# Kernel optimization log

Measured on AMD Instinct MI355X. Metric: run time of the kernel, lower is better.

## Reference

```python
import jax, jax.numpy as jnp
import numpy as np

N = 50000          # num nodes
E = 256            # expert_hidden_dim
H = 512            # hidden_dim (expert output / GNN dim)
NE = 5             # num experts: action, spatial, temporal, semantic, safety
K = 2              # top_k
GH = 128           # gating hidden dim
EDGES = 800000
L = 2              # gnn layers
TEMP = 1.0


def setup_inputs() -> dict:
    key = jax.random.key(0)
    ks = jax.random.split(key, 16)
    s = 0.02
    inp = {
        "text": jax.random.normal(ks[0], (N, E), jnp.float32),
        "tabular": jax.random.normal(ks[1], (N, E), jnp.float32),
        "structured": jax.random.normal(ks[2], (N, E), jnp.float32),
        "edge_index": jax.random.randint(ks[3], (2, EDGES), 0, N, jnp.int64),
        # gating MLP: [3E] -> GH -> NE
        "Wg1": jax.random.normal(ks[4], (3 * E, GH), jnp.float32) * s,
        "bg1": jnp.zeros((GH,), jnp.float32),
        "Wg2": jax.random.normal(ks[5], (GH, NE), jnp.float32) * s,
        "bg2": jnp.zeros((NE,), jnp.float32),
        # 5 expert MLPs (stacked): E -> H -> H
        "We1": jax.random.normal(ks[6], (NE, E, H), jnp.float32) * s,
        "be1": jnp.zeros((NE, H), jnp.float32),
        "We2": jax.random.normal(ks[7], (NE, H, H), jnp.float32) * s,
        "be2": jnp.zeros((NE, H), jnp.float32),
        # GNN per-layer self/neighbor transforms
        "Wself": jax.random.normal(ks[8], (L, H, H), jnp.float32) * s,
        "Wnbr": jax.random.normal(ks[9], (L, H, H), jnp.float32) * s,
    }
    return inp


def _moe_gnn(text, tabular, structured, edge_index,
             Wg1, bg1, Wg2, bg2, We1, be1, We2, be2, Wself, Wnbr):
    # ---- gating: softmax over experts, top-k, renormalize ----
    combined = jnp.concatenate([text, tabular, structured], axis=-1)  # [N, 3E]
    g = jax.nn.relu(combined @ Wg1 + bg1)
    logits = (g @ Wg2 + bg2) / TEMP                                   # [N, NE]
    probs = jax.nn.softmax(logits, axis=-1)
    top_vals, top_idx = jax.lax.top_k(probs, K)                       # [N, K]
    gates = top_vals / jnp.sum(top_vals, axis=-1, keepdims=True)      # [N, K]

    # ---- expert inputs per the forward() mapping ----
    # action->tabular, spatial->structured, temporal->text, semantic->text, safety->structured
    xin = jnp.stack([tabular, structured, text, text, structured])    # [NE, N, E]

    # ---- expert MLPs (all experts computed densely, selected by gather) ----
    h1 = jax.nn.gelu(jnp.einsum('end,edh->enh', xin, We1) + be1[:, None, :])
    eout = jnp.einsum('enh,eho->eno', h1, We2) + be2[:, None, :]      # [NE, N, H]

    # ---- gather-dispatch-scatter: weighted sum of top-k expert outputs ----
    sel = eout[top_idx, jnp.arange(N)[:, None], :]                    # [N, K, H]
    node_feats = jnp.sum(gates[..., None] * sel, axis=1)              # [N, H]

    # ---- GNN message passing over edge list ----
    src, dst = edge_index[0], edge_index[1]
    h = node_feats
    for l in range(L):
        msg = jax.ops.segment_sum((h @ Wnbr[l])[src], dst, num_segments=N)
        h = jax.nn.relu(h @ Wself[l] + msg)
    return h


def reference(text, tabular, structured, edge_index,
              Wg1, bg1, Wg2, bg2, We1, be1, We2, be2, Wself, Wnbr):
    return _moe_gnn(text, tabular, structured, edge_index,
                    Wg1, bg1, Wg2, bg2, We1, be1, We2, be2, Wself, Wnbr)
```

## Files before the change

### kernel.cpp

```cpp
#include <hip/hip_runtime.h>
#include <hip/hip_bf16.h>

#define NNODE 50000
#define M_PAD 50048
#define EDIM  256
#define HDIM  512
#define NEXP  5
#define GHID  128
#define NEDGE 800000
#define SLOTCAP 101504
#define MAXT_ALL 792
#define MAXT_R   396

typedef __attribute__((ext_vector_type(8))) short  short8;
typedef __attribute__((ext_vector_type(4))) float  float4v;
typedef __attribute__((ext_vector_type(4))) unsigned short ushort4v;

typedef __attribute__((address_space(1))) const unsigned int gas_u32;
typedef __attribute__((address_space(3))) unsigned int       las_u32;

__device__ __forceinline__ void gl_lds16(const unsigned short* g, unsigned short* l) {
    __builtin_amdgcn_global_load_lds((gas_u32*)g, (las_u32*)l, 16, 0, 0);
}
__device__ __forceinline__ unsigned short f2b(float f) {
    unsigned u = __builtin_bit_cast(unsigned, f);
    u += 0x7FFFu + ((u >> 16) & 1u);
    return (unsigned short)(u >> 16);
}
__device__ __forceinline__ float b2f(unsigned short h) {
    unsigned u = ((unsigned)h) << 16;
    return __builtin_bit_cast(float, u);
}
__device__ __forceinline__ float fast_tanh(float y) {
    float ay = fabsf(y);
    float e  = __expf(-2.0f * ay);
    float t  = (1.0f - e) / (1.0f + e);
    return (y < 0.0f) ? -t : t;
}
__device__ __forceinline__ float gelu_tanh(float x) {
    float inner = 0.7978845608028654f * (x + 0.044715f * x * x * x);
    return 0.5f * x * (1.0f + fast_tanh(inner));
}

__global__ void wtrans(const float* __restrict__ in, unsigned short* __restrict__ out,
                       int B, int R, int C) {
    int total = B * R * C;
    for (int i = blockIdx.x * blockDim.x + threadIdx.x; i < total; i += gridDim.x * blockDim.x) {
        int rc  = R * C;
        int b   = i / rc;
        int rem = i - b * rc;
        int c   = rem / R;
        int r   = rem - c * R;
        out[i] = f2b(in[(size_t)b * rc + (size_t)r * C + c]);
    }
}
__global__ void wtrans_k(const float* __restrict__ in, unsigned short* __restrict__ out,
                         int R, int C, int ldo, int ko) {
    int total = R * C;
    for (int i = blockIdx.x * blockDim.x + threadIdx.x; i < total; i += gridDim.x * blockDim.x) {
        int c = i / R;
        int r = i - c * R;
        out[(size_t)c * ldo + ko + r] = f2b(in[(size_t)r * C + c]);
    }
}
__global__ void wtrans2(const float* __restrict__ in, unsigned short* __restrict__ oh,
                        unsigned short* __restrict__ ol, int R, int C) {
    int total = R * C;
    for (int i = blockIdx.x * blockDim.x + threadIdx.x; i < total; i += gridDim.x * blockDim.x) {
        int c = i / R;
        int r = i - c * R;
        float f = in[(size_t)r * C + c];
        unsigned short h = f2b(f);
        oh[i] = h;
        ol[i] = f2b(f - b2f(h));
    }
}

__global__ __launch_bounds__(256) void gate128(
    const float* __restrict__ xtxt, const float* __restrict__ xtab, const float* __restrict__ xstr,
    const unsigned short* __restrict__ Bh, const unsigned short* __restrict__ Blo,
    const float* __restrict__ bg1, float* __restrict__ g) {
    __shared__ unsigned short Ash[128 * 64];
    __shared__ unsigned short Asl[128 * 64];
    __shared__ unsigned short Bsh[128 * 64];
    __shared__ unsigned short Bsl[128 * 64];
    const int t = threadIdx.x, w = t >> 6, lane = t & 63;
    const int ln = lane & 15, q = lane >> 4;
    const int wm = (w >> 1) * 64, wn = (w & 1) * 64;
    const int rb = w * 8 + (lane >> 3), kg = lane & 7;
    const int koff = (kg ^ (rb & 7)) * 8;
    const float* xs[3] = { xtxt, xtab, xstr };
    const unsigned short* Bgh = Bh  + (size_t)rb * 768 + koff;
    const unsigned short* Bgl = Blo + (size_t)rb * 768 + koff;
    unsigned short* Blh = &Bsh[rb * 64 + kg * 8];
    unsigned short* Bll = &Bsl[rb * 64 + kg * 8];
    float4v acc[4][4];
#pragma unroll
    for (int i = 0; i < 4; ++i)
#pragma unroll
        for (int j = 0; j < 4; ++j) acc[i][j] = (float4v){0.f, 0.f, 0.f, 0.f};

    for (int kt = 0; kt < 768; kt += 64) {
        const float* xp = xs[kt >> 8];
        const int kloc = kt & 255;
        __syncthreads();
#pragma unroll
        for (int it = 0; it < 4; ++it) {
            int row = blockIdx.y * 128 + rb + 32 * it;
            union { short8 v; unsigned short s[8]; } ph, pl;
            if (row < NNODE) {
                const float* sp = xp + (size_t)row * EDIM + kloc + koff;
                float4v a0 = *(const float4v*)sp;
                float4v a1 = *(const float4v*)(sp + 4);
#pragma unroll
                for (int c = 0; c < 4; ++c) {
                    unsigned short h0 = f2b(a0[c]);
                    ph.s[c] = h0; pl.s[c] = f2b(a0[c] - b2f(h0));
                    unsigned short h1 = f2b(a1[c]);
                    ph.s[4 + c] = h1; pl.s[4 + c] = f2b(a1[c] - b2f(h1));
                }
            } else {
#pragma unroll
                for (int c = 0; c < 8; ++c) { ph.s[c] = 0; pl.s[c] = 0; }
            }
            *(short8*)&Ash[(rb + 32 * it) * 64 + kg * 8] = ph.v;
            *(short8*)&Asl[(rb + 32 * it) * 64 + kg * 8] = pl.v;
            gl_lds16(Bgh + (size_t)it * 32 * 768 + kt, Blh + it * 32 * 64);
            gl_lds16(Bgl + (size_t)it * 32 * 768 + kt, Bll + it * 32 * 64);
        }
        __syncthreads();
#pragma unroll
        for (int kk = 0; kk < 2; ++kk) {
            short8 ah[4], al[4], bh[4], bl[4];
#pragma unroll
            for (int i = 0; i < 4; ++i) {
                int off = (wm + 16 * i + ln) * 64 + (((kk * 4 + q) ^ (ln & 7)) * 8);
                ah[i] = *(const short8*)&Ash[off];
                al[i] = *(const short8*)&Asl[off];
            }
#pragma unroll
            for (int j = 0; j < 4; ++j) {
                int off = (wn + 16 * j + ln) * 64 + (((kk * 4 + q) ^ (ln & 7)) * 8);
                bh[j] = *(const short8*)&Bsh[off];
                bl[j] = *(const short8*)&Bsl[off];
            }
#pragma unroll
            for (int i = 0; i < 4; ++i)
#pragma unroll
                for (int j = 0; j < 4; ++j) {
                    acc[i][j] = __builtin_amdgcn_mfma_f32_16x16x32_bf16(ah[i], bh[j], acc[i][j], 0, 0, 0);
                    acc[i][j] = __builtin_amdgcn_mfma_f32_16x16x32_bf16(ah[i], bl[j], acc[i][j], 0, 0, 0);
                    acc[i][j] = __builtin_amdgcn_mfma_f32_16x16x32_bf16(al[i], bh[j], acc[i][j], 0, 0, 0);
                }
        }
    }
    const int gm0 = blockIdx.y * 128 + wm;
#pragma unroll
    for (int i = 0; i < 4; ++i)
#pragma unroll
        for (int j = 0; j < 4; ++j) {
            int gn = wn + 16 * j + ln;
            float bc = bg1[gn];
#pragma unroll
            for (int r = 0; r < 4; ++r) {
                int gm = gm0 + 16 * i + q * 4 + r;
                g[(size_t)gm * GHID + gn] = fmaxf(acc[i][j][r] + bc, 0.f);
            }
        }
}

__global__ __launch_bounds__(256) void gating(
    const float* __restrict__ g, const float* __restrict__ Wg2, const float* __restrict__ bg2,
    float* __restrict__ gates, int* __restrict__ esel) {
    int wv = threadIdx.x >> 6, lane = threadIdx.x & 63;
    int n = blockIdx.x * 4 + wv;
    float p[NEXP];
    float g1 = g[(size_t)n * GHID + lane];
    float g2 = g[(size_t)n * GHID + 64 + lane];
#pragma unroll
    for (int e = 0; e < NEXP; ++e)
        p[e] = g1 * Wg2[lane * NEXP + e] + g2 * Wg2[(64 + lane) * NEXP + e];
#pragma unroll
    for (int off = 32; off > 0; off >>= 1)
#pragma unroll
        for (int e = 0; e < NEXP; ++e) p[e] += __shfl_xor(p[e], off, 64);
    if (lane == 0) {
        float l[NEXP], mx = -1e30f;
#pragma unroll
        for (int e = 0; e < NEXP; ++e) { l[e] = p[e] + bg2[e]; mx = fmaxf(mx, l[e]); }
        float pr[NEXP], s = 0.f;
#pragma unroll
        for (int e = 0; e < NEXP; ++e) { pr[e] = expf(l[e] - mx); s += pr[e]; }
#pragma unroll
        for (int e = 0; e < NEXP; ++e) pr[e] /= s;
        int i0 = 0;
#pragma unroll
        for (int e = 1; e < NEXP; ++e) if (pr[e] > pr[i0]) i0 = e;
        int i1 = -1;
#pragma unroll
        for (int e = 0; e < NEXP; ++e) if (e != i0 && (i1 < 0 || pr[e] > pr[i1])) i1 = e;
        float v0 = pr[i0], v1 = pr[i1], s2 = v0 + v1;
        gates[2 * n]     = v0 / s2;
        gates[2 * n + 1] = v1 / s2;
        esel[2 * n]      = i0;
        esel[2 * n + 1]  = i1;
    }
}

__global__ __launch_bounds__(256) void slot_count(const int* __restrict__ esel,
                                                  int* __restrict__ slotcnt) {
    __shared__ int h[10];
    if (threadIdx.x < 10) h[threadIdx.x] = 0;
    __syncthreads();
    int n = blockIdx.x * 256 + threadIdx.x;
    if (n < NNODE) {
        atomicAdd(&h[esel[2 * n] * 2 + 0], 1);
        atomicAdd(&h[esel[2 * n + 1] * 2 + 1], 1);
    }
    __syncthreads();
    if (threadIdx.x < 10) atomicAdd(&slotcnt[threadIdx.x], h[threadIdx.x]);
}
__global__ void seg_plan(const int* __restrict__ slotcnt, int* __restrict__ cursor,
                         int* __restrict__ header, int2* __restrict__ meta_all,
                         int2* __restrict__ meta_r0, int2* __restrict__ meta_r1) {
    if (threadIdx.x == 0 && blockIdx.x == 0) {
        int base = 0, ta = 0, t0 = 0, t1 = 0;
        for (int s = 0; s < 10; ++s) {
            cursor[s] = base;
            int nt = (slotcnt[s] + 127) >> 7;
            for (int k = 0; k < nt; ++k) {
                int2 m; m.x = s; m.y = base + k * 128;
                meta_all[ta++] = m;
                if (s & 1) meta_r1[t1++] = m; else meta_r0[t0++] = m;
            }
            base += nt * 128;
        }
        header[0] = ta; header[1] = t0; header[2] = t1;
    }
}
__global__ __launch_bounds__(256) void slot_fill(
    const int* __restrict__ esel, const float* __restrict__ gates, int* __restrict__ cursor,
    int* __restrict__ rowlist, float* __restrict__ gateval) {
    __shared__ int h[10], base[10];
    if (threadIdx.x < 10) h[threadIdx.x] = 0;
    __syncthreads();
    int n = blockIdx.x * 256 + threadIdx.x;
    int s0 = 0, s1 = 0, p0 = 0, p1 = 0;
    bool on = (n < NNODE);
    if (on) {
        s0 = esel[2 * n] * 2;
        s1 = esel[2 * n + 1] * 2 + 1;
        p0 = atomicAdd(&h[s0], 1);
        p1 = atomicAdd(&h[s1], 1);
    }
    __syncthreads();
    if (threadIdx.x < 10) base[threadIdx.x] = atomicAdd(&cursor[threadIdx.x], h[threadIdx.x]);
    __syncthreads();
    if (on) {
        int q0 = base[s0] + p0, q1 = base[s1] + p1;
        rowlist[q0] = n; gateval[q0] = gates[2 * n];
        rowlist[q1] = n; gateval[q1] = gates[2 * n + 1];
    }
}

__global__ __launch_bounds__(256) void gemm_moe1(
    const float* __restrict__ xtab, const float* __restrict__ xstr, const float* __restrict__ xtxt,
    const unsigned short* __restrict__ We1t, const float* __restrict__ be1,
    const int* __restrict__ header, const int2* __restrict__ meta,
    const int* __restrict__ rowlist, unsigned short* __restrict__ h1) {
    if ((int)blockIdx.y >= header[0]) return;
    __shared__ unsigned short As[128 * 64];
    __shared__ unsigned short Bs[128 * 64];
    int2 mt = meta[blockIdx.y];
    const int eid = mt.x >> 1, rowbase = mt.y;
    const float* xf = (eid == 0) ? xtab : ((eid == 1 || eid == 4) ? xstr : xtxt);
    const int t = threadIdx.x, w = t >> 6, lane = t & 63;
    const int ln = lane & 15, q = lane >> 4;
    const int wm = (w >> 1) * 64, wn = (w & 1) * 64;
    const int rb = w * 8 + (lane >> 3), kg = lane & 7;
    const int koff = (kg ^ (rb & 7)) * 8;
    int rows[4];
#pragma unroll
    for (int it = 0; it < 4; ++it) {
        int rr = rowlist[rowbase + rb + 32 * it];
        rows[it] = (rr < 0) ? 0 : rr;
    }
    const unsigned short* Bg = We1t + (size_t)eid * HDIM * EDIM
                             + (size_t)(blockIdx.x * 128 + rb) * EDIM + koff;
    unsigned short* Bl = &Bs[rb * 64 + kg * 8];
    float4v acc[4][4];
#pragma unroll
    for (int i = 0; i < 4; ++i)
#pragma unroll
        for (int j = 0; j < 4; ++j) acc[i][j] = (float4v){0.f, 0.f, 0.f, 0.f};

    for (int kt = 0; kt < EDIM; kt += 64) {
        __syncthreads();
#pragma unroll
        for (int it = 0; it < 4; ++it) {
            const float* sp = xf + (size_t)rows[it] * EDIM + kt + koff;
            float4v a0 = *(const float4v*)sp;
            float4v a1 = *(const float4v*)(sp + 4);
            union { short8 v; unsigned short s[8]; } pk;
#pragma unroll
            for (int c = 0; c < 4; ++c) { pk.s[c] = f2b(a0[c]); pk.s[4 + c] = f2b(a1[c]); }
            *(short8*)&As[(rb + 32 * it) * 64 + kg * 8] = pk.v;
            gl_lds16(Bg + (size_t)it * 32 * EDIM + kt, Bl + it * 32 * 64);
        }
        __syncthreads();
#pragma unroll
        for (int kk = 0; kk < 2; ++kk) {
            short8 af[4], bf[4];
#pragma unroll
            for (int i = 0; i < 4; ++i)
                af[i] = *(const short8*)&As[(wm + 16 * i + ln) * 64 + (((kk * 4 + q) ^ (ln & 7)) * 8)];
#pragma unroll
            for (int j = 0; j < 4; ++j)
                bf[j] = *(const short8*)&Bs[(wn + 16 * j + ln) * 64 + (((kk * 4 + q) ^ (ln & 7)) * 8)];
#pragma unroll
            for (int i = 0; i < 4; ++i)
#pragma unroll
                for (int j = 0; j < 4; ++j)
                    acc[i][j] = __builtin_amdgcn_mfma_f32_16x16x32_bf16(af[i], bf[j], acc[i][j], 0, 0, 0);
        }
    }
    const int gn0 = blockIdx.x * 128 + wn;
#pragma unroll
    for (int i = 0; i < 4; ++i)
#pragma unroll
        for (int j = 0; j < 4; ++j) {
            int gn = gn0 + 16 * j + ln;
            float bc = be1[eid * HDIM + gn];
#pragma unroll
            for (int r = 0; r < 4; ++r) {
                int slot = rowbase + wm + 16 * i + q * 4 + r;
                h1[(size_t)slot * HDIM + gn] = f2b(gelu_tanh(acc[i][j][r] + bc));
            }
        }
}

template<int RMW>
__global__ __launch_bounds__(256) void gemm_moe2(
    const unsigned short* __restrict__ h1, const unsigned short* __restrict__ We2t,
    const float* __restrict__ be2, const int* __restrict__ header,
    const int2* __restrict__ meta, const int* __restrict__ rowlist,
    const float* __restrict__ gateval, unsigned short* __restrict__ nf) {
    if ((int)blockIdx.y >= header[RMW ? 2 : 1]) return;
    __shared__ unsigned short As[128 * 64];
    __shared__ unsigned short Bs[128 * 64];
    int2 mt = meta[blockIdx.y];
    const int eid = mt.x >> 1, rowbase = mt.y;
    const int t = threadIdx.x, w = t >> 6, lane = t & 63;
    const int ln = lane & 15, q = lane >> 4;
    const int wm = (w >> 1) * 64, wn = (w & 1) * 64;
    const int rb = w * 8 + (lane >> 3), kg = lane & 7;
    const int koff = (kg ^ (rb & 7)) * 8;
    const unsigned short* Ag = h1 + (size_t)(rowbase + rb) * HDIM + koff;
    const unsigned short* Bg = We2t + (size_t)eid * HDIM * HDIM
                             + (size_t)(blockIdx.x * 128 + rb) * HDIM + koff;
    unsigned short* Al = &As[rb * 64 + kg * 8];
    unsigned short* Bl = &Bs[rb * 64 + kg * 8];
    float4v acc[4][4];
#pragma unroll
    for (int i = 0; i < 4; ++i)
#pragma unroll
        for (int j = 0; j < 4; ++j) acc[i][j] = (float4v){0.f, 0.f, 0.f, 0.f};

    for (int kt = 0; kt < HDIM; kt += 64) {
        __syncthreads();
#pragma unroll
        for (int it = 0; it < 4; ++it) {
            gl_lds16(Ag + (size_t)it * 32 * HDIM + kt, Al + it * 32 * 64);
            gl_lds16(Bg + (size_t)it * 32 * HDIM + kt, Bl + it * 32 * 64);
        }
        __syncthreads();
#pragma unroll
        for (int kk = 0; kk < 2; ++kk) {
            short8 af[4], bf[4];
#pragma unroll
            for (int i = 0; i < 4; ++i)
                af[i] = *(const short8*)&As[(wm + 16 * i + ln) * 64 + (((kk * 4 + q) ^ (ln & 7)) * 8)];
#pragma unroll
            for (int j = 0; j < 4; ++j)
                bf[j] = *(const short8*)&Bs[(wn + 16 * j + ln) * 64 + (((kk * 4 + q) ^ (ln & 7)) * 8)];
#pragma unroll
            for (int i = 0; i < 4; ++i)
#pragma unroll
                for (int j = 0; j < 4; ++j)
                    acc[i][j] = __builtin_amdgcn_mfma_f32_16x16x32_bf16(af[i], bf[j], acc[i][j], 0, 0, 0);
        }
    }
    const int gn0 = blockIdx.x * 128 + wn;
#pragma unroll
    for (int i = 0; i < 4; ++i)
#pragma unroll
        for (int r = 0; r < 4; ++r) {
            int slot = rowbase + wm + 16 * i + q * 4 + r;
            int node = rowlist[slot];
            if (node >= 0) {
                float gt = gateval[slot];
#pragma unroll
                for (int j = 0; j < 4; ++j) {
                    int gn = gn0 + 16 * j + ln;
                    size_t o = (size_t)node * HDIM + gn;
                    float v = gt * (acc[i][j][r] + be2[eid * HDIM + gn]);
                    nf[o] = RMW ? f2b(b2f(nf[o]) + v) : f2b(v);
                }
            }
        }
}

template<int FINAL>
__global__ __launch_bounds__(256) void gemm_gnn(
    const unsigned short* __restrict__ A0, const unsigned short* __restrict__ A1,
    const unsigned short* __restrict__ Bt, unsigned short* __restrict__ Cb,
    float* __restrict__ Cf) {
    __shared__ unsigned short As[128 * 64];
    __shared__ unsigned short Bs[128 * 64];
    const int t = threadIdx.x, w = t >> 6, lane = t & 63;
    const int ln = lane & 15, q = lane >> 4;
    const int wm = (w >> 1) * 64, wn = (w & 1) * 64;
    const int rb = w * 8 + (lane >> 3), kg = lane & 7;
    const int koff = (kg ^ (rb & 7)) * 8;
    const unsigned short* Ag0 = A0 + (size_t)(blockIdx.y * 128 + rb) * HDIM + koff;
    const unsigned short* Ag1 = A1 + (size_t)(blockIdx.y * 128 + rb) * HDIM + koff;
    const unsigned short* Bg  = Bt + (size_t)(blockIdx.x * 128 + rb) * 1024 + koff;
    unsigned short* Al = &As[rb * 64 + kg * 8];
    unsigned short* Bl = &Bs[rb * 64 + kg * 8];
    float4v acc[4][4];
#pragma unroll
    for (int i = 0; i < 4; ++i)
#pragma unroll
        for (int j = 0; j < 4; ++j) acc[i][j] = (float4v){0.f, 0.f, 0.f, 0.f};

    for (int kt = 0; kt < 1024; kt += 64) {
        __syncthreads();
#pragma unroll
        for (int it = 0; it < 4; ++it) {
            const unsigned short* asrc = (kt < HDIM)
                ? (Ag0 + (size_t)it * 32 * HDIM + kt)
                : (Ag1 + (size_t)it * 32 * HDIM + (kt - HDIM));
            gl_lds16(asrc, Al + it * 32 * 64);
            gl_lds16(Bg + (size_t)it * 32 * 1024 + kt, Bl + it * 32 * 64);
        }
        __syncthreads();
#pragma unroll
        for (int kk = 0; kk < 2; ++kk) {
            short8 af[4], bf[4];
#pragma unroll
            for (int i = 0; i < 4; ++i)
                af[i] = *(const short8*)&As[(wm + 16 * i + ln) * 64 + (((kk * 4 + q) ^ (ln & 7)) * 8)];
#pragma unroll
            for (int j = 0; j < 4; ++j)
                bf[j] = *(const short8*)&Bs[(wn + 16 * j + ln) * 64 + (((kk * 4 + q) ^ (ln & 7)) * 8)];
#pragma unroll
            for (int i = 0; i < 4; ++i)
#pragma unroll
                for (int j = 0; j < 4; ++j)
                    acc[i][j] = __builtin_amdgcn_mfma_f32_16x16x32_bf16(af[i], bf[j], acc[i][j], 0, 0, 0);
        }
    }
    const int gm0 = blockIdx.y * 128 + wm;
    const int gn0 = blockIdx.x * 128 + wn;
#pragma unroll
    for (int i = 0; i < 4; ++i)
#pragma unroll
        for (int j = 0; j < 4; ++j) {
            int gn = gn0 + 16 * j + ln;
#pragma unroll
            for (int r = 0; r < 4; ++r) {
                int gm = gm0 + 16 * i + q * 4 + r;
                float v = fmaxf(acc[i][j][r], 0.f);
                if (FINAL) {
                    if (gm < NNODE) Cf[(size_t)gm * HDIM + gn] = v;
                } else {
                    Cb[(size_t)gm * HDIM + gn] = f2b(v);
                }
            }
        }
}

__global__ void hist_kernel(const int* __restrict__ dst, int* __restrict__ deg) {
    int i = blockIdx.x * blockDim.x + threadIdx.x;
    if (i < NEDGE) atomicAdd(&deg[dst[i]], 1);
}
__global__ void scan_block(const int* __restrict__ in, int* __restrict__ incl,
                           int* __restrict__ bsum, int n) {
    __shared__ int s[256];
    int i = blockIdx.x * 256 + threadIdx.x;
    s[threadIdx.x] = (i < n) ? in[i] : 0;
    __syncthreads();
    for (int off = 1; off < 256; off <<= 1) {
        int t = (threadIdx.x >= (unsigned)off) ? s[threadIdx.x - off] : 0;
        __syncthreads();
        s[threadIdx.x] += t;
        __syncthreads();
    }
    if (i < n) incl[i] = s[threadIdx.x];
    if (bsum != nullptr && threadIdx.x == 255) bsum[blockIdx.x] = s[255];
}
__global__ void scan_fix(const int* __restrict__ incl, const int* __restrict__ deg,
                         const int* __restrict__ bscan, int* __restrict__ rowstart,
                         int* __restrict__ ecur) {
    int i = blockIdx.x * blockDim.x + threadIdx.x;
    if (i < NNODE) {
        int b = i >> 8;
        int add = (b > 0) ? bscan[b - 1] : 0;
        int st = incl[i] - deg[i] + add;
        rowstart[i] = st;
        ecur[i] = st;
    }
}
__global__ void fill_csr(const int* __restrict__ src, const int* __restrict__ dst,
                         int* __restrict__ ecur, int* __restrict__ srcs) {
    int e = blockIdx.x * blockDim.x + threadIdx.x;
    if (e < NEDGE) {
        int pos = atomicAdd(&ecur[dst[e]], 1);
        srcs[pos] = src[e];
    }
}

__global__ __launch_bounds__(256) void msg_sum_b(
    const unsigned short* __restrict__ h, const int* __restrict__ rowstart,
    const int* __restrict__ deg, const int* __restrict__ srcs,
    unsigned short* __restrict__ agg) {
    __shared__ float sm[4][HDIM];
    int n = blockIdx.x;
    int wv = threadIdx.x >> 6, lane = threadIdx.x & 63;
    int st = rowstart[n], d = deg[n];
    float acc[8] = {0.f,0.f,0.f,0.f,0.f,0.f,0.f,0.f};
    for (int t = wv; t < d; t += 4) {
        int s = srcs[st + t];
        short8 v = *(const short8*)(h + (size_t)s * HDIM + lane * 8);
#pragma unroll
        for (int c = 0; c < 8; ++c) acc[c] += b2f((unsigned short)v[c]);
    }
#pragma unroll
    for (int c = 0; c < 8; ++c) sm[wv][lane * 8 + c] = acc[c];
    __syncthreads();
    if (threadIdx.x < 128) {
        int c0 = threadIdx.x * 4;
        ushort4v o;
#pragma unroll
        for (int c = 0; c < 4; ++c)
            o[c] = f2b(sm[0][c0 + c] + sm[1][c0 + c] + sm[2][c0 + c] + sm[3][c0 + c]);
        *(ushort4v*)(agg + (size_t)n * HDIM + c0) = o;
    }
}

extern "C" void kernel_launch(void* const* d_in, const int* in_sizes, int n_in,
                              void* d_out, int out_size, void* d_ws, size_t ws_size,
                              hipStream_t stream) {
    (void)in_sizes; (void)n_in; (void)out_size; (void)ws_size;
    const float* text       = (const float*)d_in[0];
    const float* tabular    = (const float*)d_in[1];
    const float* structured = (const float*)d_in[2];
    const int*   e_in       = (const int*)d_in[3];
    const float* Wg1  = (const float*)d_in[4];
    const float* bg1  = (const float*)d_in[5];
    const float* Wg2  = (const float*)d_in[6];
    const float* bg2  = (const float*)d_in[7];
    const float* We1  = (const float*)d_in[8];
    const float* be1  = (const float*)d_in[9];
    const float* We2  = (const float*)d_in[10];
    const float* be2  = (const float*)d_in[11];
    const float* Wself = (const float*)d_in[12];
    const float* Wnbr  = (const float*)d_in[13];
    const int* src = e_in;
    const int* dst = e_in + NEDGE;
    float* dout = (float*)d_out;

    char* w = (char*)d_ws;
    auto alloc = [&](size_t bytes) { char* p = w; w += (bytes + 511) & ~(size_t)511; return p; };
    const size_t SZ_H = (size_t)M_PAD * HDIM * 2;
    unsigned short* We1t  = (unsigned short*)alloc((size_t)NEXP * HDIM * EDIM * 2);
    unsigned short* We2t  = (unsigned short*)alloc((size_t)NEXP * HDIM * HDIM * 2);
    unsigned short* Wcat0 = (unsigned short*)alloc((size_t)HDIM * 1024 * 2);
    unsigned short* Wcat1 = (unsigned short*)alloc((size_t)HDIM * 1024 * 2);
    unsigned short* Wg1h  = (unsigned short*)alloc((size_t)GHID * 768 * 2);
    unsigned short* Wg1l  = (unsigned short*)alloc((size_t)GHID * 768 * 2);
    float* gates    = (float*)alloc((size_t)NNODE * 2 * 4);
    int*   esel     = (int*)alloc((size_t)NNODE * 2 * 4);
    int*   slotcnt  = (int*)alloc(16 * 4);
    int*   scursor  = (int*)alloc(16 * 4);
    int*   header   = (int*)alloc(16 * 4);
    int2*  meta_all = (int2*)alloc((size_t)MAXT_ALL * 8);
    int2*  meta_r0  = (int2*)alloc((size_t)MAXT_R * 8);
    int2*  meta_r1  = (int2*)alloc((size_t)MAXT_R * 8);
    int*   rowlist  = (int*)alloc((size_t)SLOTCAP * 4);
    float* gateval  = (float*)alloc((size_t)SLOTCAP * 4);
    int*   deg      = (int*)alloc((size_t)NNODE * 4);
    int*   incl     = (int*)alloc((size_t)NNODE * 4);
    int*   bsum     = (int*)alloc(1024 * 4);
    int*   bscan    = (int*)alloc(1024 * 4);
    int*   rowstart = (int*)alloc((size_t)NNODE * 4);
    int*   ecur     = (int*)alloc((size_t)NNODE * 4);
    int*   srcs     = (int*)alloc((size_t)NEDGE * 4);
    unsigned short* nfb = (unsigned short*)alloc(SZ_H);
    char* regA = alloc((size_t)M_PAD * GHID * 4 > SZ_H ? (size_t)M_PAD * GHID * 4 : SZ_H);
    float*          gbuf = (float*)regA;
    unsigned short* aggb = (unsigned short*)regA;
    char* regB = alloc((size_t)SLOTCAP * HDIM * 2);
    unsigned short* h1c = (unsigned short*)regB;
    unsigned short* hb  = (unsigned short*)regB;

    wtrans  <<<512, 256, 0, stream>>>(We1, We1t, NEXP, EDIM, HDIM);
    wtrans  <<<512, 256, 0, stream>>>(We2, We2t, NEXP, HDIM, HDIM);
    wtrans_k<<<512, 256, 0, stream>>>(Wself,               Wcat0, HDIM, HDIM, 1024, 0);
    wtrans_k<<<512, 256, 0, stream>>>(Wnbr,                Wcat0, HDIM, HDIM, 1024, 512);
    wtrans_k<<<512, 256, 0, stream>>>(Wself + HDIM * HDIM, Wcat1, HDIM, HDIM, 1024, 0);
    wtrans_k<<<512, 256, 0, stream>>>(Wnbr  + HDIM * HDIM, Wcat1, HDIM, HDIM, 1024, 512);
    wtrans2 <<<512, 256, 0, stream>>>(Wg1, Wg1h, Wg1l, 3 * EDIM, GHID);

    hipMemsetAsync(slotcnt, 0, 16 * 4, stream);
    hipMemsetAsync(rowlist, 0xFF, (size_t)SLOTCAP * 4, stream);
    hipMemsetAsync(deg, 0, (size_t)NNODE * 4, stream);

    gate128<<<dim3(1, M_PAD / 128), 256, 0, stream>>>(text, tabular, structured,
                                                      Wg1h, Wg1l, bg1, gbuf);
    gating<<<NNODE / 4, 256, 0, stream>>>(gbuf, Wg2, bg2, gates, esel);

    slot_count<<<(NNODE + 255) / 256, 256, 0, stream>>>(esel, slotcnt);
    seg_plan<<<1, 64, 0, stream>>>(slotcnt, scursor, header, meta_all, meta_r0, meta_r1);
    slot_fill<<<(NNODE + 255) / 256, 256, 0, stream>>>(esel, gates, scursor, rowlist, gateval);

    gemm_moe1<<<dim3(HDIM / 128, MAXT_ALL), 256, 0, stream>>>(
        tabular, structured, text, We1t, be1, header, meta_all, rowlist, h1c);
    gemm_moe2<0><<<dim3(HDIM / 128, MAXT_R), 256, 0, stream>>>(
        h1c, We2t, be2, header, meta_r0, rowlist, gateval, nfb);
    gemm_moe2<1><<<dim3(HDIM / 128, MAXT_R), 256, 0, stream>>>(
        h1c, We2t, be2, header, meta_r1, rowlist, gateval, nfb);

    const int NB = (NNODE + 255) / 256;
    hist_kernel<<<(NEDGE + 255) / 256, 256, 0, stream>>>(dst, deg);
    scan_block<<<NB, 256, 0, stream>>>(deg, incl, bsum, NNODE);
    scan_block<<<1, 256, 0, stream>>>(bsum, bscan, nullptr, NB);
    scan_fix<<<NB, 256, 0, stream>>>(incl, deg, bscan, rowstart, ecur);
    fill_csr<<<(NEDGE + 255) / 256, 256, 0, stream>>>(src, dst, ecur, srcs);

    msg_sum_b<<<NNODE, 256, 0, stream>>>(nfb, rowstart, deg, srcs, aggb);
    gemm_gnn<0><<<dim3(HDIM / 128, M_PAD / 128), 256, 0, stream>>>(nfb, aggb, Wcat0, hb, nullptr);

    msg_sum_b<<<NNODE, 256, 0, stream>>>(hb, rowstart, deg, srcs, aggb);
    gemm_gnn<1><<<dim3(HDIM / 128, M_PAD / 128), 256, 0, stream>>>(hb, aggb, Wcat1, nullptr, dout);
}
```

Measured before the change: 1.122 ms.

## Assign one wavefront per node in neighbor aggregation with shuffled index loads

The neighbor-sum kernel now gives each wavefront its own destination node instead of splitting one node across four waves and reducing through shared memory. Source indices are read cooperatively, 64 at a time, and broadcast with shuffles, and four gathered rows are issued per iteration to keep more loads in flight. This removes the LDS reduction, the block barrier and the per-edge scalar index loads. The trade-off is possible load imbalance across waves when node degrees vary.

```diff
diff --git a/kernel.cpp b/kernel.cpp
--- a/kernel.cpp
+++ b/kernel.cpp
@@ -520,32 +520,44 @@
     }
 }
 
-__global__ __launch_bounds__(256) void msg_sum_b(
+__global__ __launch_bounds__(256) void msg_sum_w(
     const unsigned short* __restrict__ h, const int* __restrict__ rowstart,
     const int* __restrict__ deg, const int* __restrict__ srcs,
     unsigned short* __restrict__ agg) {
-    __shared__ float sm[4][HDIM];
-    int n = blockIdx.x;
-    int wv = threadIdx.x >> 6, lane = threadIdx.x & 63;
-    int st = rowstart[n], d = deg[n];
+    const int wv = threadIdx.x >> 6, lane = threadIdx.x & 63;
+    const int n = blockIdx.x * 4 + wv;
+    const int st = rowstart[n], d = deg[n];
     float acc[8] = {0.f,0.f,0.f,0.f,0.f,0.f,0.f,0.f};
-    for (int t = wv; t < d; t += 4) {
-        int s = srcs[st + t];
-        short8 v = *(const short8*)(h + (size_t)s * HDIM + lane * 8);
-#pragma unroll
-        for (int c = 0; c < 8; ++c) acc[c] += b2f((unsigned short)v[c]);
-    }
-#pragma unroll
-    for (int c = 0; c < 8; ++c) sm[wv][lane * 8 + c] = acc[c];
-    __syncthreads();
-    if (threadIdx.x < 128) {
-        int c0 = threadIdx.x * 4;
-        ushort4v o;
-#pragma unroll
-        for (int c = 0; c < 4; ++c)
-            o[c] = f2b(sm[0][c0 + c] + sm[1][c0 + c] + sm[2][c0 + c] + sm[3][c0 + c]);
-        *(ushort4v*)(agg + (size_t)n * HDIM + c0) = o;
-    }
+    const unsigned short* hp = h + (size_t)lane * 8;
+    for (int cb = 0; cb < d; cb += 64) {
+        int cnt = d - cb; if (cnt > 64) cnt = 64;
+        int sidx = (cb + lane < d) ? srcs[st + cb + lane] : 0;
+        int t = 0;
+        for (; t + 4 <= cnt; t += 4) {
+            int s0 = __shfl(sidx, t,     64);
+            int s1 = __shfl(sidx, t + 1, 64);
+            int s2 = __shfl(sidx, t + 2, 64);
+            int s3 = __shfl(sidx, t + 3, 64);
+            short8 v0 = *(const short8*)(hp + (size_t)s0 * HDIM);
+            short8 v1 = *(const short8*)(hp + (size_t)s1 * HDIM);
+            short8 v2 = *(const short8*)(hp + (size_t)s2 * HDIM);
+            short8 v3 = *(const short8*)(hp + (size_t)s3 * HDIM);
+#pragma unroll
+            for (int c = 0; c < 8; ++c)
+                acc[c] += (b2f((unsigned short)v0[c]) + b2f((unsigned short)v1[c]))
+                        + (b2f((unsigned short)v2[c]) + b2f((unsigned short)v3[c]));
+        }
+        for (; t < cnt; ++t) {
+            int s = __shfl(sidx, t, 64);
+            short8 v = *(const short8*)(hp + (size_t)s * HDIM);
+#pragma unroll
+            for (int c = 0; c < 8; ++c) acc[c] += b2f((unsigned short)v[c]);
+        }
+    }
+    union { short8 v; unsigned short s[8]; } o;
+#pragma unroll
+    for (int c = 0; c < 8; ++c) o.s[c] = f2b(acc[c]);
+    *(short8*)(agg + (size_t)n * HDIM + lane * 8) = o.v;
 }
 
 extern "C" void kernel_launch(void* const* d_in, const int* in_sizes, int n_in,
@@ -638,9 +650,9 @@
     scan_fix<<<NB, 256, 0, stream>>>(incl, deg, bscan, rowstart, ecur);
     fill_csr<<<(NEDGE + 255) / 256, 256, 0, stream>>>(src, dst, ecur, srcs);
 
-    msg_sum_b<<<NNODE, 256, 0, stream>>>(nfb, rowstart, deg, srcs, aggb);
+    msg_sum_w<<<NNODE / 4, 256, 0, stream>>>(nfb, rowstart, deg, srcs, aggb);
     gemm_gnn<0><<<dim3(HDIM / 128, M_PAD / 128), 256, 0, stream>>>(nfb, aggb, Wcat0, hb, nullptr);
 
-    msg_sum_b<<<NNODE, 256, 0, stream>>>(hb, rowstart, deg, srcs, aggb);
+    msg_sum_w<<<NNODE / 4, 256, 0, stream>>>(hb, rowstart, deg, srcs, aggb);
     gemm_gnn<1><<<dim3(HDIM / 128, M_PAD / 128), 256, 0, stream>>>(hb, aggb, Wcat1, nullptr, dout);
 }
```

After: 1.124 ms. No clear change (+0.2%).

## Split CSR by source half and gather column slices for cache-local message sums

Applied to the files above, without the earlier changes.

Builds the CSR keyed by (destination, source-half), so each destination's neighbour list is split by whether the source id falls in the lower or upper half of the nodes. The message-sum kernel is rewritten so each block handles a 64-column slice for a chunk of 128 nodes. It processes lower-half sources for all nodes first, then upper-half sources, keeping partial sums in shared memory. The aim is to shrink the working set of gathered rows so it stays resident in cache. The trade-off is 2-byte per-lane scalar gathers in place of 16-byte vector loads, plus a larger scan over 2N entries.

```diff
diff --git a/kernel.cpp b/kernel.cpp
--- a/kernel.cpp
+++ b/kernel.cpp
@@ -11,6 +11,9 @@
 #define SLOTCAP 101504
 #define MAXT_ALL 792
 #define MAXT_R   396
+#define HALFN 25000
+#define MSG_CHUNK 128
+#define MSG_CHUNKS ((NNODE + MSG_CHUNK - 1) / MSG_CHUNK)
 
 typedef __attribute__((ext_vector_type(8))) short  short8;
 typedef __attribute__((ext_vector_type(4))) float  float4v;
@@ -480,9 +483,10 @@
         }
 }
 
-__global__ void hist_kernel(const int* __restrict__ dst, int* __restrict__ deg) {
+__global__ void hist2(const int* __restrict__ src, const int* __restrict__ dst,
+                      int* __restrict__ deg2) {
     int i = blockIdx.x * blockDim.x + threadIdx.x;
-    if (i < NEDGE) atomicAdd(&deg[dst[i]], 1);
+    if (i < NEDGE) atomicAdd(&deg2[2 * dst[i] + (src[i] >= HALFN)], 1);
 }
 __global__ void scan_block(const int* __restrict__ in, int* __restrict__ incl,
                            int* __restrict__ bsum, int n) {
@@ -499,52 +503,84 @@
     if (i < n) incl[i] = s[threadIdx.x];
     if (bsum != nullptr && threadIdx.x == 255) bsum[blockIdx.x] = s[255];
 }
-__global__ void scan_fix(const int* __restrict__ incl, const int* __restrict__ deg,
-                         const int* __restrict__ bscan, int* __restrict__ rowstart,
-                         int* __restrict__ ecur) {
+__global__ void scan_lvl2(const int* __restrict__ in, int* __restrict__ out, int n) {
+    __shared__ int s[1024];
+    int i = threadIdx.x;
+    s[i] = (i < n) ? in[i] : 0;
+    __syncthreads();
+    for (int off = 1; off < 1024; off <<= 1) {
+        int t = (i >= (unsigned)off) ? s[i - off] : 0;
+        __syncthreads();
+        s[i] += t;
+        __syncthreads();
+    }
+    if (i < n) out[i] = s[i];
+}
+__global__ void scan_fix2(const int* __restrict__ incl, const int* __restrict__ deg2,
+                          const int* __restrict__ bscan, int* __restrict__ rowstart2,
+                          int* __restrict__ ecur2, int n) {
     int i = blockIdx.x * blockDim.x + threadIdx.x;
-    if (i < NNODE) {
+    if (i < n) {
         int b = i >> 8;
         int add = (b > 0) ? bscan[b - 1] : 0;
-        int st = incl[i] - deg[i] + add;
-        rowstart[i] = st;
-        ecur[i] = st;
-    }
-}
-__global__ void fill_csr(const int* __restrict__ src, const int* __restrict__ dst,
-                         int* __restrict__ ecur, int* __restrict__ srcs) {
+        int st = incl[i] - deg2[i] + add;
+        rowstart2[i] = st;
+        ecur2[i] = st;
+    }
+}
+__global__ void fill_csr2(const int* __restrict__ src, const int* __restrict__ dst,
+                          int* __restrict__ ecur2, int* __restrict__ srcs) {
     int e = blockIdx.x * blockDim.x + threadIdx.x;
     if (e < NEDGE) {
-        int pos = atomicAdd(&ecur[dst[e]], 1);
-        srcs[pos] = src[e];
-    }
-}
-
-__global__ __launch_bounds__(256) void msg_sum_b(
-    const unsigned short* __restrict__ h, const int* __restrict__ rowstart,
-    const int* __restrict__ deg, const int* __restrict__ srcs,
+        int s = src[e];
+        int pos = atomicAdd(&ecur2[2 * dst[e] + (s >= HALFN)], 1);
+        srcs[pos] = s;
+    }
+}
+
+__global__ __launch_bounds__(256) void msg_sum_s(
+    const unsigned short* __restrict__ h, const int* __restrict__ rowstart2,
+    const int* __restrict__ deg2, const int* __restrict__ srcs,
     unsigned short* __restrict__ agg) {
-    __shared__ float sm[4][HDIM];
-    int n = blockIdx.x;
-    int wv = threadIdx.x >> 6, lane = threadIdx.x & 63;
-    int st = rowstart[n], d = deg[n];
-    float acc[8] = {0.f,0.f,0.f,0.f,0.f,0.f,0.f,0.f};
-    for (int t = wv; t < d; t += 4) {
-        int s = srcs[st + t];
-        short8 v = *(const short8*)(h + (size_t)s * HDIM + lane * 8);
-#pragma unroll
-        for (int c = 0; c < 8; ++c) acc[c] += b2f((unsigned short)v[c]);
-    }
-#pragma unroll
-    for (int c = 0; c < 8; ++c) sm[wv][lane * 8 + c] = acc[c];
-    __syncthreads();
-    if (threadIdx.x < 128) {
-        int c0 = threadIdx.x * 4;
-        ushort4v o;
-#pragma unroll
-        for (int c = 0; c < 4; ++c)
-            o[c] = f2b(sm[0][c0 + c] + sm[1][c0 + c] + sm[2][c0 + c] + sm[3][c0 + c]);
-        *(ushort4v*)(agg + (size_t)n * HDIM + c0) = o;
+    __shared__ float part[4][32][64];
+    const int wv = threadIdx.x >> 6, lane = threadIdx.x & 63;
+    const int slice = blockIdx.x & 7;
+    const int chunk = blockIdx.x >> 3;
+    const int nbase = chunk * MSG_CHUNK + wv * 32;
+    const unsigned short* hp = h + (size_t)slice * 64 + lane;
+#pragma unroll 1
+    for (int ph = 0; ph < 2; ++ph) {
+#pragma unroll 1
+        for (int k = 0; k < 32; ++k) {
+            int n = nbase + k;
+            if (n >= NNODE) break;
+            int st = rowstart2[2 * n + ph];
+            int d  = deg2[2 * n + ph];
+            float a = (ph == 0) ? 0.f : part[wv][k][lane];
+            int t = 0;
+            for (; t + 8 <= d; t += 8) {
+                int s0 = srcs[st + t],     s1 = srcs[st + t + 1];
+                int s2 = srcs[st + t + 2], s3 = srcs[st + t + 3];
+                int s4 = srcs[st + t + 4], s5 = srcs[st + t + 5];
+                int s6 = srcs[st + t + 6], s7 = srcs[st + t + 7];
+                unsigned short v0 = hp[(size_t)s0 * HDIM], v1 = hp[(size_t)s1 * HDIM];
+                unsigned short v2 = hp[(size_t)s2 * HDIM], v3 = hp[(size_t)s3 * HDIM];
+                unsigned short v4 = hp[(size_t)s4 * HDIM], v5 = hp[(size_t)s5 * HDIM];
+                unsigned short v6 = hp[(size_t)s6 * HDIM], v7 = hp[(size_t)s7 * HDIM];
+                a += ((b2f(v0) + b2f(v1)) + (b2f(v2) + b2f(v3)))
+                   + ((b2f(v4) + b2f(v5)) + (b2f(v6) + b2f(v7)));
+            }
+            for (; t < d; ++t) {
+                int s = srcs[st + t];
+                a += b2f(hp[(size_t)s * HDIM]);
+            }
+            if (ph == 0) {
+                part[wv][k][lane] = a;
+            } else {
+                __builtin_nontemporal_store(
+                    f2b(a), agg + (size_t)n * HDIM + slice * 64 + lane);
+            }
+        }
     }
 }
 
@@ -589,12 +625,12 @@
     int2*  meta_r1  = (int2*)alloc((size_t)MAXT_R * 8);
     int*   rowlist  = (int*)alloc((size_t)SLOTCAP * 4);
     float* gateval  = (float*)alloc((size_t)SLOTCAP * 4);
-    int*   deg      = (int*)alloc((size_t)NNODE * 4);
-    int*   incl     = (int*)alloc((size_t)NNODE * 4);
+    int*   deg2     = (int*)alloc((size_t)2 * NNODE * 4);
+    int*   incl     = (int*)alloc((size_t)2 * NNODE * 4);
     int*   bsum     = (int*)alloc(1024 * 4);
     int*   bscan    = (int*)alloc(1024 * 4);
-    int*   rowstart = (int*)alloc((size_t)NNODE * 4);
-    int*   ecur     = (int*)alloc((size_t)NNODE * 4);
+    int*   rowstart2= (int*)alloc((size_t)2 * NNODE * 4);
+    int*   ecur2    = (int*)alloc((size_t)2 * NNODE * 4);
     int*   srcs     = (int*)alloc((size_t)NEDGE * 4);
     unsigned short* nfb = (unsigned short*)alloc(SZ_H);
     char* regA = alloc((size_t)M_PAD * GHID * 4 > SZ_H ? (size_t)M_PAD * GHID * 4 : SZ_H);
@@ -614,7 +650,7 @@
 
     hipMemsetAsync(slotcnt, 0, 16 * 4, stream);
     hipMemsetAsync(rowlist, 0xFF, (size_t)SLOTCAP * 4, stream);
-    hipMemsetAsync(deg, 0, (size_t)NNODE * 4, stream);
+    hipMemsetAsync(deg2, 0, (size_t)2 * NNODE * 4, stream);
 
     gate128<<<dim3(1, M_PAD / 128), 256, 0, stream>>>(text, tabular, structured,
                                                       Wg1h, Wg1l, bg1, gbuf);
@@ -631,16 +667,17 @@
     gemm_moe2<1><<<dim3(HDIM / 128, MAXT_R), 256, 0, stream>>>(
         h1c, We2t, be2, header, meta_r1, rowlist, gateval, nfb);
 
-    const int NB = (NNODE + 255) / 256;
-    hist_kernel<<<(NEDGE + 255) / 256, 256, 0, stream>>>(dst, deg);
-    scan_block<<<NB, 256, 0, stream>>>(deg, incl, bsum, NNODE);
-    scan_block<<<1, 256, 0, stream>>>(bsum, bscan, nullptr, NB);
-    scan_fix<<<NB, 256, 0, stream>>>(incl, deg, bscan, rowstart, ecur);
-    fill_csr<<<(NEDGE + 255) / 256, 256, 0, stream>>>(src, dst, ecur, srcs);
-
-    msg_sum_b<<<NNODE, 256, 0, stream>>>(nfb, rowstart, deg, srcs, aggb);
+    const int N2  = 2 * NNODE;
+    const int NB2 = (N2 + 255) / 256;
+    hist2<<<(NEDGE + 255) / 256, 256, 0, stream>>>(src, dst, deg2);
+    scan_block<<<NB2, 256, 0, stream>>>(deg2, incl, bsum, N2);
+    scan_lvl2<<<1, 1024, 0, stream>>>(bsum, bscan, NB2);
+    scan_fix2<<<NB2, 256, 0, stream>>>(incl, deg2, bscan, rowstart2, ecur2, N2);
+    fill_csr2<<<(NEDGE + 255) / 256, 256, 0, stream>>>(src, dst, ecur2, srcs);
+
+    msg_sum_s<<<8 * MSG_CHUNKS, 256, 0, stream>>>(nfb, rowstart2, deg2, srcs, aggb);
     gemm_gnn<0><<<dim3(HDIM / 128, M_PAD / 128), 256, 0, stream>>>(nfb, aggb, Wcat0, hb, nullptr);
 
-    msg_sum_b<<<NNODE, 256, 0, stream>>>(hb, rowstart, deg, srcs, aggb);
+    msg_sum_s<<<8 * MSG_CHUNKS, 256, 0, stream>>>(hb, rowstart2, deg2, srcs, aggb);
     gemm_gnn<1><<<dim3(HDIM / 128, M_PAD / 128), 256, 0, stream>>>(hb, aggb, Wcat1, nullptr, dout);
 }
```

Result: slower. 1.961 ms (+74.8%).
